# Kernel tuning notes

Hardware: AMD Instinct MI355X
Metric: run time of the kernel (lower is better)

Reference implementation:

```python
import jax
import jax.numpy as jnp
import numpy as np
from jax import lax


def hard_sigmoid(x):
    # keras hard_sigmoid: clip(0.2*x + 0.5, 0, 1)
    return jnp.clip(0.2 * x + 0.5, 0.0, 1.0)


def setup_inputs() -> dict:
    key = jax.random.key(0)
    k1, k2, k3 = jax.random.split(key, 3)
    B, T, H, W, C = 8, 16, 256, 256, 3
    F, K = 36, 5
    states_in = jax.random.normal(k1, (B, T, H, W, C), dtype=jnp.float32)
    Wx = jax.random.normal(k2, (K, K, C, 4 * F), dtype=jnp.float32) * 0.05
    Wh = jax.random.normal(k3, (K, K, F, 4 * F), dtype=jnp.float32) * 0.05
    b = jnp.zeros((4 * F,), dtype=jnp.float32)
    return {"states_in": states_in, "Wx": Wx, "Wh": Wh, "b": b}


def reference(states_in, Wx, Wh, b):
    # ConvLSTM2D(filters=36, kernel=5, strides=(4,4), padding='valid') + Flatten
    B, T, H, W, C = states_in.shape
    F = Wh.shape[2]
    dn = ("NHWC", "HWIO", "NHWC")

    # Precompute strided input convs for all timesteps in one big conv (batched over B*T)
    x = states_in.reshape(B * T, H, W, C)
    xconv = lax.conv_general_dilated(x, Wx, (4, 4), "VALID", dimension_numbers=dn) + b
    Ho, Wo = xconv.shape[1], xconv.shape[2]  # (256-5)//4+1 = 63
    xconv = xconv.reshape(B, T, Ho, Wo, 4 * F).transpose(1, 0, 2, 3, 4)  # time-major

    def step(carry, xt):
        h, c = carry
        # recurrent conv: strides 1, SAME padding (keras ConvLSTM2D behavior)
        hconv = lax.conv_general_dilated(h, Wh, (1, 1), "SAME", dimension_numbers=dn)
        z = xt + hconv
        zi, zf, zc, zo = jnp.split(z, 4, axis=-1)  # keras gate order i,f,c,o
        i = hard_sigmoid(zi)
        f = hard_sigmoid(zf)
        o = hard_sigmoid(zo)
        c_new = f * c + i * jnp.tanh(zc)
        h_new = o * jnp.tanh(c_new)
        return (h_new, c_new), None

    h0 = jnp.zeros((B, Ho, Wo, F), dtype=states_in.dtype)
    (h, c), _ = lax.scan(step, (h0, h0), xconv)
    return h.reshape(B, -1)  # Flatten -> (B, Ho*Wo*F)
```

## Files before the change

### kernel.cpp

```cpp
#include <hip/hip_runtime.h>


typedef _Float16 f16;
typedef __attribute__((ext_vector_type(8))) _Float16 f16x8;
typedef __attribute__((ext_vector_type(4))) float f32x4;

#define TPB 256

#define H_SH_OFF   0
#define X_SH_OFF   28944
#define W2_SH_OFF  43136
#define W_SH_OFF   100736
#define Z_SH_OFF   28944
#define LDS_BYTES  160640

#define WHP_GRAN_PER_SLICE 1872
#define W_BUF_USH 14976

union Cv8 { ushort4 u4[2]; uint4 q; f16x8 h8; };
union Cvh { f16 h; ushort u; };
union Cv2 { f16 h[2]; uint u; };

__device__ inline f16x8 ld8_lds(const ushort* p) {
  Cv8 c; c.u4[0] = *(const ushort4*)p; c.u4[1] = *(const ushort4*)(p + 4);
  return c.h8;
}
__device__ inline f16x8 ld16_lds(const ushort* p) {
  Cv8 c; c.q = *(const uint4*)p; return c.h8;
}
__device__ inline ushort f2us(float v) { Cvh c; c.h = (f16)v; return c.u; }

typedef const __attribute__((address_space(1))) uint guint;
typedef __attribute__((address_space(3))) uint luint;
__device__ inline void gload_lds16(const void* gp, void* lp) {
  __builtin_amdgcn_global_load_lds((guint*)gp, (luint*)lp, 16, 0, 0);
}

__device__ inline float tanh_fast(float x) {
  float e = __expf(2.f * x);
  return 1.f - 2.f * __builtin_amdgcn_rcpf(e + 1.f);
}

__global__ void prep_weights(const float* __restrict__ Wx, const float* __restrict__ Wh,
                             const float* __restrict__ bb,
                             ushort* __restrict__ whp, ushort* __restrict__ wxp,
                             float* __restrict__ bperm) {
  int i = blockIdx.x * 256 + threadIdx.x;
  if (i < 149760) {
    int kk = i % 104; int rest = i / 104;
    int np = rest % 144; int s = rest / 144;
    int kh = s >> 1, hf = s & 1;
    int k = hf * 96 + kk;
    float v = 0.f;
    if (kk < 96 && k < 180) {
      int kw = k / 36, c = k - kw * 36;
      int fq = np >> 4, g = (np >> 2) & 3, fr = np & 3;
      int n = g * 36 + fq * 4 + fr;
      v = Wh[(((kh * 5 + kw) * 36 + c) * 144) + n];
    }
    whp[i] = f2us(v);
  } else if (i < 178560) {
    int e = i - 149760;
    int kk2 = e % 40; int rest = e / 40;
    int np = rest % 144; int kh2 = rest / 144;
    float v = 0.f;
    if (kk2 < 15) {
      int kw = kk2 / 3, cin = kk2 - kw * 3;
      int fq = np >> 4, g = (np >> 2) & 3, fr = np & 3;
      int n = g * 36 + fq * 4 + fr;
      v = Wx[(((kh2 * 5 + kw) * 3 + cin) * 144) + n];
    }
    wxp[e] = f2us(v);
  } else if (i < 178704) {
    int np = i - 178560;
    int fq = np >> 4, g = (np >> 2) & 3, fr = np & 3;
    bperm[np] = bb[g * 36 + fq * 4 + fr];
  }
}

template<int S, int FQ0>
__device__ void x_chunks(f32x4 (&acc)[4][5], const ushort* x_sh, const ushort* w2_sh,
                         int mh, int lane) {
  const int l16 = lane & 15, lg = lane >> 4;
#pragma unroll
  for (int kh2 = 0; kh2 < 5; ++kh2) {
    f16x8 a[4];
#pragma unroll
    for (int r = 0; r < 4; ++r)
      a[r] = ld8_lds(x_sh + (mh * 4 + kh2) * 788 + (r * 16 + l16) * 12 + lg * 8);
#pragma unroll
    for (int s = 0; s < S; ++s) {
      f16x8 bf = ld16_lds(w2_sh + (kh2 * 144 + (FQ0 + s) * 16 + l16) * 40 + lg * 8);
#pragma unroll
      for (int r = 0; r < 4; ++r)
        acc[r][s] = __builtin_amdgcn_mfma_f32_16x16x32_f16(a[r], bf, acc[r][s], 0, 0, 0);
    }
  }
}

template<int S, int FQ0>
__device__ void h_chunks(f32x4 (&acc)[4][5], const ushort* h_sh, const ushort* wbuf,
                         int kh, int hf, int mh, int lane) {
  const int l16 = lane & 15, lg = lane >> 4;
  const ushort* hrow = h_sh + (mh + kh) * 2412;
#pragma unroll
  for (int cc = 0; cc < 3; ++cc) {
    const int k0 = hf * 96 + cc * 32;
    f16x8 a[4];
#pragma unroll
    for (int r = 0; r < 4; ++r)
      a[r] = ld8_lds(hrow + (r * 16 + l16) * 36 + k0 + lg * 8);
#pragma unroll
    for (int s = 0; s < S; ++s) {
      f16x8 bf = ld16_lds(wbuf + ((FQ0 + s) * 16 + l16) * 104 + cc * 32 + lg * 8);
#pragma unroll
      for (int r = 0; r < 4; ++r)
        acc[r][s] = __builtin_amdgcn_mfma_f32_16x16x32_f16(a[r], bf, acc[r][s], 0, 0, 0);
    }
  }
}

template<int S, int FQ0>
__device__ void z_write(const f32x4 (&acc)[4][5], float* z_sh, int mh, int lane) {
  const int l16 = lane & 15, lg = lane >> 4;
#pragma unroll
  for (int r = 0; r < 4; ++r)
#pragma unroll
    for (int s = 0; s < S; ++s)
#pragma unroll
      for (int j = 0; j < 4; ++j)
        z_sh[(mh * 64 + r * 16 + lg * 4 + j) * 148 + (FQ0 + s) * 16 + l16] = acc[r][s][j];
}

__device__ inline void stage_wh_slice(const ushort* whp, int slice, ushort* dstbuf, int tid) {
  const uint4* src = (const uint4*)whp + (size_t)slice * WHP_GRAN_PER_SLICE;
#pragma unroll
  for (int k = 0; k < 8; ++k) {
    int g = tid + k * 256;
    if (g < WHP_GRAN_PER_SLICE)
      gload_lds16(src + g, (char*)dstbuf + (size_t)g * 16);
  }
}

__global__ __launch_bounds__(TPB, 1)
void convlstm_step(const float* __restrict__ x_all, int t,
                   const f16* __restrict__ h_prev, f16* __restrict__ h_next,
                   float* __restrict__ c_st,
                   const ushort* __restrict__ whp, const ushort* __restrict__ wxp,
                   const float* __restrict__ bperm,
                   float* __restrict__ out, int flags) {
  extern __shared__ char smem[];
  ushort* h_sh  = (ushort*)(smem + H_SH_OFF);
  ushort* x_sh  = (ushort*)(smem + X_SH_OFF);
  ushort* w2_sh = (ushort*)(smem + W2_SH_OFF);
  ushort* w_sh  = (ushort*)(smem + W_SH_OFF);
  float*  z_sh  = (float*)(smem + Z_SH_OFF);

  const int tid = threadIdx.x;
  const int lane = tid & 63, wave = tid >> 6;
  const int mh = wave >> 1, nh = wave & 1;
  const int y0 = blockIdx.x * 2, b = blockIdx.y;
  const bool first = (flags & 1) != 0, last = (flags & 2) != 0;

  {
    const uint4* src = (const uint4*)wxp;
#pragma unroll
    for (int k = 0; k < 15; ++k) {
      int g = tid + k * 256;
      if (g < 3600) gload_lds16(src + g, (char*)w2_sh + (size_t)g * 16);
    }
  }
  if (!first) stage_wh_slice(whp, 0, w_sh, tid);

  {
    const float* xrow0 = x_all + (size_t)(b * 16 + t) * 196608;
    uint* xs32 = (uint*)x_sh;
#pragma unroll
    for (int k = 0; k < 7; ++k) {
      int g = tid + k * 256;
      if (g < 1728) {
        int row = g / 192, e = g - row * 192;
        int yi = y0 * 4 + row;
        float4 v = make_float4(0.f, 0.f, 0.f, 0.f);
        if (yi < 256) v = *(const float4*)(xrow0 + yi * 768 + e * 4);
        Cv2 c0, c1;
        c0.h[0] = (f16)v.x; c0.h[1] = (f16)v.y;
        c1.h[0] = (f16)v.z; c1.h[1] = (f16)v.w;
        xs32[row * 394 + e * 2]     = c0.u;
        xs32[row * 394 + e * 2 + 1] = c1.u;
      }
    }
    if (tid < 90) {
      int row = tid / 10, u = 384 + (tid - (tid / 10) * 10);
      xs32[row * 394 + u] = 0;
    }
  }
  if (!first) {
    const uint2* src = (const uint2*)h_prev;
    uint2* hs = (uint2*)h_sh;
#pragma unroll
    for (int k = 0; k < 15; ++k) {
      int g = tid + k * 256;
      if (g < 3618) {
        int row = g / 603, u2 = g - row * 603;
        int hy = y0 - 2 + row;
        uint2 val = make_uint2(0, 0);
        if (hy >= 0 && hy < 63 && u2 >= 18 && u2 < 585)
          val = src[(size_t)(b * 63 + hy) * 567 + (u2 - 18)];
        hs[g] = val;
      }
    }
  }
  __syncthreads();

  f32x4 acc[4][5];
#pragma unroll
  for (int r = 0; r < 4; ++r)
#pragma unroll
    for (int s = 0; s < 5; ++s) acc[r][s] = (f32x4)(0.f);

  if (nh == 0) x_chunks<5, 0>(acc, x_sh, w2_sh, mh, lane);
  else         x_chunks<4, 5>(acc, x_sh, w2_sh, mh, lane);

  if (!first) {
#pragma unroll 1
    for (int s = 0; s < 10; ++s) {
      if (s < 9)
        stage_wh_slice(whp, s + 1, w_sh + ((s + 1) & 1) * W_BUF_USH, tid);
      const ushort* wbuf = w_sh + (s & 1) * W_BUF_USH;
      if (nh == 0) h_chunks<5, 0>(acc, h_sh, wbuf, s >> 1, s & 1, mh, lane);
      else         h_chunks<4, 5>(acc, h_sh, wbuf, s >> 1, s & 1, mh, lane);
      __syncthreads();
    }
  }

  __syncthreads();
  if (nh == 0) z_write<5, 0>(acc, z_sh, mh, lane);
  else         z_write<4, 5>(acc, z_sh, mh, lane);
  __syncthreads();

#pragma unroll 1
  for (int it = 0; it < 18; ++it) {
    int u = tid + it * 256;
    int x_sub = u / 36, f = u - x_sub * 36;
    int x = x_sub & 63, y = y0 + (x_sub >> 6);
    if (x < 63 && y < 63) {
      int cb = (f >> 2) * 16 + (f & 3);
      const float* zr = z_sh + x_sub * 148;
      float zi = zr[cb]      + bperm[cb];
      float zf = zr[cb + 4]  + bperm[cb + 4];
      float zc = zr[cb + 8]  + bperm[cb + 8];
      float zo = zr[cb + 12] + bperm[cb + 12];
      float gi = fminf(fmaxf(0.2f * zi + 0.5f, 0.f), 1.f);
      float gf = fminf(fmaxf(0.2f * zf + 0.5f, 0.f), 1.f);
      float go = fminf(fmaxf(0.2f * zo + 0.5f, 0.f), 1.f);
      float tc = tanh_fast(zc);
      size_t idx = (size_t)((b * 63 + y) * 63 + x) * 36 + f;
      float cold = first ? 0.f : c_st[idx];
      float cn = gf * cold + gi * tc;
      float hn = go * tanh_fast(cn);
      c_st[idx] = cn;
      h_next[idx] = (f16)hn;
      if (last) out[(size_t)b * 142884 + ((y * 63 + x) * 36 + f)] = hn;
    }
  }
}

extern "C" void kernel_launch(void* const* d_in, const int* in_sizes, int n_in,
                              void* d_out, int out_size, void* d_ws, size_t ws_size,
                              hipStream_t stream) {
  (void)in_sizes; (void)n_in; (void)out_size; (void)ws_size;
  const float* states = (const float*)d_in[0];
  const float* Wx = (const float*)d_in[1];
  const float* Wh = (const float*)d_in[2];
  const float* bb = (const float*)d_in[3];
  float* out = (float*)d_out;
  char* ws = (char*)d_ws;

  ushort* whp   = (ushort*)(ws + 0);
  ushort* wxp   = (ushort*)(ws + 299520);
  float*  bperm = (float*)(ws + 357120);
  f16*    hb0   = (f16*)(ws + 357696);
  f16*    hb1   = (f16*)(ws + 2643840);
  float*  c_st  = (float*)(ws + 4929984);

  hipFuncSetAttribute((const void*)convlstm_step,
                      hipFuncAttributeMaxDynamicSharedMemorySize, LDS_BYTES);

  prep_weights<<<699, 256, 0, stream>>>(Wx, Wh, bb, whp, wxp, bperm);
  for (int t = 0; t < 16; ++t) {
    int flags = (t == 0 ? 1 : 0) | (t == 15 ? 2 : 0);
    f16* hp = (t & 1) ? hb1 : hb0;
    f16* hn = (t & 1) ? hb0 : hb1;
    convlstm_step<<<dim3(32, 8), TPB, LDS_BYTES, stream>>>(
        states, t, hp, hn, c_st, whp, wxp, bperm, out, flags);
  }
}
```

Measured before the change: 614.9 us.

## Fuse all timesteps into one persistent cooperative kernel with split-K waves

Replaces the 16 per-timestep launches with a single cooperative kernel that loops over time and uses a grid-wide sync between steps. Block size doubles to 512 so two wave groups split the K reduction, and their partial accumulators are summed through LDS. The Wh staging is rebuilt as a six-chunk ring of 32-wide K chunks, the x conv switches to 16x16x16 MFMA with a tighter weight layout, and the bias is cached in LDS. This removes per-step launch overhead and idle tails, at the cost of grid-sync latency and an extra LDS reduction pass.

```diff
diff --git a/kernel.cpp b/kernel.cpp
--- a/kernel.cpp
+++ b/kernel.cpp
@@ -1,23 +1,29 @@
 #include <hip/hip_runtime.h>
+#include <hip/hip_cooperative_groups.h>
+
+namespace cg = cooperative_groups;
 
 
 typedef _Float16 f16;
+typedef __attribute__((ext_vector_type(4))) _Float16 f16x4;
 typedef __attribute__((ext_vector_type(8))) _Float16 f16x8;
 typedef __attribute__((ext_vector_type(4))) float f32x4;
 
-#define TPB 256
+#define TPB 512
 
 #define H_SH_OFF   0
 #define X_SH_OFF   28944
-#define W2_SH_OFF  43136
-#define W_SH_OFF   100736
-#define Z_SH_OFF   28944
-#define LDS_BYTES  160640
-
-#define WHP_GRAN_PER_SLICE 1872
-#define W_BUF_USH 14976
+#define RING_OFF   43136
+#define W2_SH_OFF  112256
+#define BP_OFF     141056
+#define LDS_BYTES  141632
+#define Z_SH_OFF   0
+
+#define CHUNK_USH 5760
+#define CHUNK_U4  720
 
 union Cv8 { ushort4 u4[2]; uint4 q; f16x8 h8; };
+union Cv4 { ushort4 u; f16x4 h; };
 union Cvh { f16 h; ushort u; };
 union Cv2 { f16 h[2]; uint u; };
 
@@ -27,6 +33,9 @@
 }
 __device__ inline f16x8 ld16_lds(const ushort* p) {
   Cv8 c; c.q = *(const uint4*)p; return c.h8;
+}
+__device__ inline f16x4 ld4_lds(const ushort* p) {
+  Cv4 c; c.u = *(const ushort4*)p; return c.h;
 }
 __device__ inline ushort f2us(float v) { Cvh c; c.h = (f16)v; return c.u; }
 
@@ -46,223 +55,247 @@
                              ushort* __restrict__ whp, ushort* __restrict__ wxp,
                              float* __restrict__ bperm) {
   int i = blockIdx.x * 256 + threadIdx.x;
-  if (i < 149760) {
-    int kk = i % 104; int rest = i / 104;
-    int np = rest % 144; int s = rest / 144;
-    int kh = s >> 1, hf = s & 1;
-    int k = hf * 96 + kk;
+  if (i < 172800) {
+    int j = i % 40; int rest = i / 40;
+    int np = rest % 144; int ck = rest / 144;
+    int kh = ck / 6, cc6 = ck - kh * 6;
+    int k = cc6 * 32 + j;
     float v = 0.f;
-    if (kk < 96 && k < 180) {
+    if (j < 32 && k < 180) {
       int kw = k / 36, c = k - kw * 36;
       int fq = np >> 4, g = (np >> 2) & 3, fr = np & 3;
       int n = g * 36 + fq * 4 + fr;
       v = Wh[(((kh * 5 + kw) * 36 + c) * 144) + n];
     }
     whp[i] = f2us(v);
-  } else if (i < 178560) {
-    int e = i - 149760;
-    int kk2 = e % 40; int rest = e / 40;
+  } else if (i < 187200) {
+    int e = i - 172800;
+    int j = e % 20; int rest = e / 20;
     int np = rest % 144; int kh2 = rest / 144;
     float v = 0.f;
-    if (kk2 < 15) {
-      int kw = kk2 / 3, cin = kk2 - kw * 3;
+    if (j < 15) {
+      int kw = j / 3, cin = j - kw * 3;
       int fq = np >> 4, g = (np >> 2) & 3, fr = np & 3;
       int n = g * 36 + fq * 4 + fr;
       v = Wx[(((kh2 * 5 + kw) * 3 + cin) * 144) + n];
     }
     wxp[e] = f2us(v);
-  } else if (i < 178704) {
-    int np = i - 178560;
+  } else if (i < 187344) {
+    int np = i - 187200;
     int fq = np >> 4, g = (np >> 2) & 3, fr = np & 3;
     bperm[np] = bb[g * 36 + fq * 4 + fr];
   }
 }
 
+template<int S, int FQ0, int K0, int K1>
+__device__ void x_conv(f32x4 (&acc)[4][5], const ushort* x_sh, const ushort* w2,
+                       int mh, int l16, int lg) {
+#pragma unroll
+  for (int kh2 = K0; kh2 < K1; ++kh2) {
+    f16x4 a[4];
+#pragma unroll
+    for (int r = 0; r < 4; ++r)
+      a[r] = ld4_lds(x_sh + (mh * 4 + kh2) * 788 + (r * 16 + l16) * 12 + lg * 4);
+#pragma unroll
+    for (int s = 0; s < S; ++s) {
+      f16x4 bf = ld4_lds(w2 + (kh2 * 144 + (FQ0 + s) * 16 + l16) * 20 + lg * 4);
+#pragma unroll
+      for (int r = 0; r < 4; ++r)
+        acc[r][s] = __builtin_amdgcn_mfma_f32_16x16x16f16(a[r], bf, acc[r][s], 0, 0, 0);
+    }
+  }
+}
+
 template<int S, int FQ0>
-__device__ void x_chunks(f32x4 (&acc)[4][5], const ushort* x_sh, const ushort* w2_sh,
-                         int mh, int lane) {
+__device__ void h_phase(f32x4 (&acc)[4][5], const ushort* hrow, const ushort* wbuf,
+                        int k0, int l16, int lg) {
+  f16x8 a[4];
+#pragma unroll
+  for (int r = 0; r < 4; ++r)
+    a[r] = ld8_lds(hrow + (r * 16 + l16) * 36 + k0 + lg * 8);
+#pragma unroll
+  for (int s = 0; s < S; ++s) {
+    f16x8 bf = ld16_lds(wbuf + ((FQ0 + s) * 16 + l16) * 40 + lg * 8);
+#pragma unroll
+    for (int r = 0; r < 4; ++r)
+      acc[r][s] = __builtin_amdgcn_mfma_f32_16x16x32_f16(a[r], bf, acc[r][s], 0, 0, 0);
+  }
+}
+
+template<int S, int FQ0, bool ADD>
+__device__ void z_out(const f32x4 (&acc)[4][5], float* z_sh, int mh, int l16, int lg) {
+#pragma unroll
+  for (int r = 0; r < 4; ++r)
+#pragma unroll
+    for (int s = 0; s < S; ++s)
+#pragma unroll
+      for (int j = 0; j < 4; ++j) {
+        float* p = &z_sh[(mh * 64 + r * 16 + lg * 4 + j) * 148 + (FQ0 + s) * 16 + l16];
+        if (ADD) *p += acc[r][s][j]; else *p = acc[r][s][j];
+      }
+}
+
+__global__ __launch_bounds__(TPB, 2)
+void convlstm_all(const float* __restrict__ x_all,
+                  const ushort* __restrict__ whp, const ushort* __restrict__ wxp,
+                  const float* __restrict__ bperm,
+                  f16* __restrict__ hb0, f16* __restrict__ hb1,
+                  float* __restrict__ c_st, float* __restrict__ out) {
+  extern __shared__ char smem[];
+  ushort* h_sh = (ushort*)(smem + H_SH_OFF);
+  ushort* x_sh = (ushort*)(smem + X_SH_OFF);
+  ushort* ring = (ushort*)(smem + RING_OFF);
+  ushort* w2   = (ushort*)(smem + W2_SH_OFF);
+  float*  bp_sh = (float*)(smem + BP_OFF);
+  float*  z_sh  = (float*)(smem + Z_SH_OFF);
+
+  cg::grid_group gg = cg::this_grid();
+
+  const int tid = threadIdx.x;
+  const int lane = tid & 63, w = tid >> 6;
+  const int kq = w >> 2, mh = (w >> 1) & 1, nh = w & 1;
   const int l16 = lane & 15, lg = lane >> 4;
-#pragma unroll
-  for (int kh2 = 0; kh2 < 5; ++kh2) {
-    f16x8 a[4];
-#pragma unroll
-    for (int r = 0; r < 4; ++r)
-      a[r] = ld8_lds(x_sh + (mh * 4 + kh2) * 788 + (r * 16 + l16) * 12 + lg * 8);
-#pragma unroll
-    for (int s = 0; s < S; ++s) {
-      f16x8 bf = ld16_lds(w2_sh + (kh2 * 144 + (FQ0 + s) * 16 + l16) * 40 + lg * 8);
-#pragma unroll
-      for (int r = 0; r < 4; ++r)
-        acc[r][s] = __builtin_amdgcn_mfma_f32_16x16x32_f16(a[r], bf, acc[r][s], 0, 0, 0);
-    }
-  }
-}
-
-template<int S, int FQ0>
-__device__ void h_chunks(f32x4 (&acc)[4][5], const ushort* h_sh, const ushort* wbuf,
-                         int kh, int hf, int mh, int lane) {
-  const int l16 = lane & 15, lg = lane >> 4;
-  const ushort* hrow = h_sh + (mh + kh) * 2412;
-#pragma unroll
-  for (int cc = 0; cc < 3; ++cc) {
-    const int k0 = hf * 96 + cc * 32;
-    f16x8 a[4];
-#pragma unroll
-    for (int r = 0; r < 4; ++r)
-      a[r] = ld8_lds(hrow + (r * 16 + l16) * 36 + k0 + lg * 8);
-#pragma unroll
-    for (int s = 0; s < S; ++s) {
-      f16x8 bf = ld16_lds(wbuf + ((FQ0 + s) * 16 + l16) * 104 + cc * 32 + lg * 8);
-#pragma unroll
-      for (int r = 0; r < 4; ++r)
-        acc[r][s] = __builtin_amdgcn_mfma_f32_16x16x32_f16(a[r], bf, acc[r][s], 0, 0, 0);
-    }
-  }
-}
-
-template<int S, int FQ0>
-__device__ void z_write(const f32x4 (&acc)[4][5], float* z_sh, int mh, int lane) {
-  const int l16 = lane & 15, lg = lane >> 4;
-#pragma unroll
-  for (int r = 0; r < 4; ++r)
-#pragma unroll
-    for (int s = 0; s < S; ++s)
-#pragma unroll
-      for (int j = 0; j < 4; ++j)
-        z_sh[(mh * 64 + r * 16 + lg * 4 + j) * 148 + (FQ0 + s) * 16 + l16] = acc[r][s][j];
-}
-
-__device__ inline void stage_wh_slice(const ushort* whp, int slice, ushort* dstbuf, int tid) {
-  const uint4* src = (const uint4*)whp + (size_t)slice * WHP_GRAN_PER_SLICE;
-#pragma unroll
-  for (int k = 0; k < 8; ++k) {
-    int g = tid + k * 256;
-    if (g < WHP_GRAN_PER_SLICE)
-      gload_lds16(src + g, (char*)dstbuf + (size_t)g * 16);
-  }
-}
-
-__global__ __launch_bounds__(TPB, 1)
-void convlstm_step(const float* __restrict__ x_all, int t,
-                   const f16* __restrict__ h_prev, f16* __restrict__ h_next,
-                   float* __restrict__ c_st,
-                   const ushort* __restrict__ whp, const ushort* __restrict__ wxp,
-                   const float* __restrict__ bperm,
-                   float* __restrict__ out, int flags) {
-  extern __shared__ char smem[];
-  ushort* h_sh  = (ushort*)(smem + H_SH_OFF);
-  ushort* x_sh  = (ushort*)(smem + X_SH_OFF);
-  ushort* w2_sh = (ushort*)(smem + W2_SH_OFF);
-  ushort* w_sh  = (ushort*)(smem + W_SH_OFF);
-  float*  z_sh  = (float*)(smem + Z_SH_OFF);
-
-  const int tid = threadIdx.x;
-  const int lane = tid & 63, wave = tid >> 6;
-  const int mh = wave >> 1, nh = wave & 1;
-  const int y0 = blockIdx.x * 2, b = blockIdx.y;
-  const bool first = (flags & 1) != 0, last = (flags & 2) != 0;
+  const int bid = blockIdx.x;
+  const int b = bid & 7;
+  const int y0 = (bid >> 3) * 2;
 
   {
     const uint4* src = (const uint4*)wxp;
 #pragma unroll
-    for (int k = 0; k < 15; ++k) {
-      int g = tid + k * 256;
-      if (g < 3600) gload_lds16(src + g, (char*)w2_sh + (size_t)g * 16);
-    }
-  }
-  if (!first) stage_wh_slice(whp, 0, w_sh, tid);
-
-  {
-    const float* xrow0 = x_all + (size_t)(b * 16 + t) * 196608;
-    uint* xs32 = (uint*)x_sh;
-#pragma unroll
-    for (int k = 0; k < 7; ++k) {
-      int g = tid + k * 256;
-      if (g < 1728) {
-        int row = g / 192, e = g - row * 192;
-        int yi = y0 * 4 + row;
-        float4 v = make_float4(0.f, 0.f, 0.f, 0.f);
-        if (yi < 256) v = *(const float4*)(xrow0 + yi * 768 + e * 4);
-        Cv2 c0, c1;
-        c0.h[0] = (f16)v.x; c0.h[1] = (f16)v.y;
-        c1.h[0] = (f16)v.z; c1.h[1] = (f16)v.w;
-        xs32[row * 394 + e * 2]     = c0.u;
-        xs32[row * 394 + e * 2 + 1] = c1.u;
-      }
-    }
-    if (tid < 90) {
-      int row = tid / 10, u = 384 + (tid - (tid / 10) * 10);
-      xs32[row * 394 + u] = 0;
-    }
-  }
-  if (!first) {
-    const uint2* src = (const uint2*)h_prev;
-    uint2* hs = (uint2*)h_sh;
-#pragma unroll
-    for (int k = 0; k < 15; ++k) {
-      int g = tid + k * 256;
-      if (g < 3618) {
-        int row = g / 603, u2 = g - row * 603;
-        int hy = y0 - 2 + row;
-        uint2 val = make_uint2(0, 0);
-        if (hy >= 0 && hy < 63 && u2 >= 18 && u2 < 585)
-          val = src[(size_t)(b * 63 + hy) * 567 + (u2 - 18)];
-        hs[g] = val;
-      }
-    }
-  }
-  __syncthreads();
-
-  f32x4 acc[4][5];
-#pragma unroll
-  for (int r = 0; r < 4; ++r)
-#pragma unroll
-    for (int s = 0; s < 5; ++s) acc[r][s] = (f32x4)(0.f);
-
-  if (nh == 0) x_chunks<5, 0>(acc, x_sh, w2_sh, mh, lane);
-  else         x_chunks<4, 5>(acc, x_sh, w2_sh, mh, lane);
-
-  if (!first) {
+    for (int k = 0; k < 4; ++k) {
+      int g = tid + k * 512;
+      if (g < 1800) gload_lds16(src + g, (char*)w2 + (size_t)g * 16);
+    }
+    if (tid < 144) bp_sh[tid] = bperm[tid];
+  }
+
 #pragma unroll 1
-    for (int s = 0; s < 10; ++s) {
-      if (s < 9)
-        stage_wh_slice(whp, s + 1, w_sh + ((s + 1) & 1) * W_BUF_USH, tid);
-      const ushort* wbuf = w_sh + (s & 1) * W_BUF_USH;
-      if (nh == 0) h_chunks<5, 0>(acc, h_sh, wbuf, s >> 1, s & 1, mh, lane);
-      else         h_chunks<4, 5>(acc, h_sh, wbuf, s >> 1, s & 1, mh, lane);
+  for (int t = 0; t < 16; ++t) {
+    const f16* hp = (t & 1) ? hb1 : hb0;
+    f16* hn = (t & 1) ? hb0 : hb1;
+    const bool first = (t == 0), last = (t == 15);
+
+    if (!first) {
+      const uint4* src = (const uint4*)whp;
+#pragma unroll
+      for (int k = 0; k < 6; ++k) {
+        int g = tid + k * 512;
+        if (g < 4 * CHUNK_U4) gload_lds16(src + g, (char*)ring + (size_t)g * 16);
+      }
+    }
+    {
+      const float* xr = x_all + (size_t)(b * 16 + t) * 196608;
+      uint* xs = (uint*)x_sh;
+#pragma unroll
+      for (int k = 0; k < 4; ++k) {
+        int g = tid + k * 512;
+        if (g < 1728) {
+          int row = g / 192, e = g - row * 192;
+          int yi = y0 * 4 + row;
+          float4 v = make_float4(0.f, 0.f, 0.f, 0.f);
+          if (yi < 256) v = *(const float4*)(xr + yi * 768 + e * 4);
+          Cv2 c0, c1;
+          c0.h[0] = (f16)v.x; c0.h[1] = (f16)v.y;
+          c1.h[0] = (f16)v.z; c1.h[1] = (f16)v.w;
+          xs[row * 394 + e * 2]     = c0.u;
+          xs[row * 394 + e * 2 + 1] = c1.u;
+        }
+      }
+      if (tid < 90) {
+        int row = tid / 10, u = 384 + (tid - (tid / 10) * 10);
+        xs[row * 394 + u] = 0;
+      }
+    }
+    if (!first) {
+      const uint2* src = (const uint2*)hp;
+      uint2* hs = (uint2*)h_sh;
+#pragma unroll
+      for (int k = 0; k < 8; ++k) {
+        int g = tid + k * 512;
+        if (g < 3618) {
+          int row = g / 603, u2 = g - row * 603;
+          int hy = y0 - 2 + row;
+          uint2 val = make_uint2(0, 0);
+          if (hy >= 0 && hy < 63 && u2 >= 18 && u2 < 585)
+            val = src[(size_t)(b * 63 + hy) * 567 + (u2 - 18)];
+          hs[g] = val;
+        }
+      }
+    }
+    __syncthreads();
+
+    f32x4 acc[4][5];
+#pragma unroll
+    for (int r = 0; r < 4; ++r)
+#pragma unroll
+      for (int s = 0; s < 5; ++s) acc[r][s] = (f32x4)(0.f);
+
+    if (nh == 0) { if (kq == 0) x_conv<5, 0, 0, 3>(acc, x_sh, w2, mh, l16, lg);
+                   else         x_conv<5, 0, 3, 5>(acc, x_sh, w2, mh, l16, lg); }
+    else         { if (kq == 0) x_conv<4, 5, 0, 3>(acc, x_sh, w2, mh, l16, lg);
+                   else         x_conv<4, 5, 3, 5>(acc, x_sh, w2, mh, l16, lg); }
+
+    if (!first) {
+#pragma unroll 1
+      for (int q = 0; q < 5; ++q) {
+        const ushort* hrow = h_sh + (mh + q) * 2412;
+#pragma unroll
+        for (int r3 = 0; r3 < 3; ++r3) {
+          int nc = 6 * q + 2 * r3 + 4;
+          if (nc < 30) {
+            const uint4* src = (const uint4*)whp + (size_t)nc * CHUNK_U4;
+            char* dst = (char*)ring + ((2 * r3 + 4) % 6) * (CHUNK_USH * 2);
+#pragma unroll
+            for (int k = 0; k < 3; ++k) {
+              int g = tid + k * 512;
+              if (g < 2 * CHUNK_U4) gload_lds16(src + g, dst + (size_t)g * 16);
+            }
+          }
+          const int cc6 = 2 * r3 + kq;
+          const ushort* wbuf = ring + cc6 * CHUNK_USH;
+          if (nh == 0) h_phase<5, 0>(acc, hrow, wbuf, cc6 * 32, l16, lg);
+          else         h_phase<4, 5>(acc, hrow, wbuf, cc6 * 32, l16, lg);
+          __syncthreads();
+        }
+      }
+    } else {
       __syncthreads();
     }
-  }
-
-  __syncthreads();
-  if (nh == 0) z_write<5, 0>(acc, z_sh, mh, lane);
-  else         z_write<4, 5>(acc, z_sh, mh, lane);
-  __syncthreads();
+
+    if (kq == 0) { if (nh == 0) z_out<5, 0, false>(acc, z_sh, mh, l16, lg);
+                   else         z_out<4, 5, false>(acc, z_sh, mh, l16, lg); }
+    __syncthreads();
+    if (kq == 1) { if (nh == 0) z_out<5, 0, true>(acc, z_sh, mh, l16, lg);
+                   else         z_out<4, 5, true>(acc, z_sh, mh, l16, lg); }
+    __syncthreads();
 
 #pragma unroll 1
-  for (int it = 0; it < 18; ++it) {
-    int u = tid + it * 256;
-    int x_sub = u / 36, f = u - x_sub * 36;
-    int x = x_sub & 63, y = y0 + (x_sub >> 6);
-    if (x < 63 && y < 63) {
-      int cb = (f >> 2) * 16 + (f & 3);
-      const float* zr = z_sh + x_sub * 148;
-      float zi = zr[cb]      + bperm[cb];
-      float zf = zr[cb + 4]  + bperm[cb + 4];
-      float zc = zr[cb + 8]  + bperm[cb + 8];
-      float zo = zr[cb + 12] + bperm[cb + 12];
-      float gi = fminf(fmaxf(0.2f * zi + 0.5f, 0.f), 1.f);
-      float gf = fminf(fmaxf(0.2f * zf + 0.5f, 0.f), 1.f);
-      float go = fminf(fmaxf(0.2f * zo + 0.5f, 0.f), 1.f);
-      float tc = tanh_fast(zc);
-      size_t idx = (size_t)((b * 63 + y) * 63 + x) * 36 + f;
-      float cold = first ? 0.f : c_st[idx];
-      float cn = gf * cold + gi * tc;
-      float hn = go * tanh_fast(cn);
-      c_st[idx] = cn;
-      h_next[idx] = (f16)hn;
-      if (last) out[(size_t)b * 142884 + ((y * 63 + x) * 36 + f)] = hn;
-    }
+    for (int it = 0; it < 9; ++it) {
+      int u = tid + it * 512;
+      int x_sub = u / 36, f = u - x_sub * 36;
+      int x = x_sub & 63, y = y0 + (x_sub >> 6);
+      if (x < 63 && y < 63) {
+        int cb = (f >> 2) * 16 + (f & 3);
+        const float* zr = z_sh + x_sub * 148;
+        float zi = zr[cb]      + bp_sh[cb];
+        float zf = zr[cb + 4]  + bp_sh[cb + 4];
+        float zc = zr[cb + 8]  + bp_sh[cb + 8];
+        float zo = zr[cb + 12] + bp_sh[cb + 12];
+        float gi = fminf(fmaxf(0.2f * zi + 0.5f, 0.f), 1.f);
+        float gf = fminf(fmaxf(0.2f * zf + 0.5f, 0.f), 1.f);
+        float go = fminf(fmaxf(0.2f * zo + 0.5f, 0.f), 1.f);
+        float tc = tanh_fast(zc);
+        size_t idx = (size_t)((b * 63 + y) * 63 + x) * 36 + f;
+        float cold = first ? 0.f : c_st[idx];
+        float cn = gf * cold + gi * tc;
+        float hnv = go * tanh_fast(cn);
+        c_st[idx] = cn;
+        hn[idx] = (f16)hnv;
+        if (last) out[(size_t)b * 142884 + ((y * 63 + x) * 36 + f)] = hnv;
+      }
+    }
+
+    if (!last) { __threadfence(); gg.sync(); }
   }
 }
 
@@ -278,21 +311,20 @@
   char* ws = (char*)d_ws;
 
   ushort* whp   = (ushort*)(ws + 0);
-  ushort* wxp   = (ushort*)(ws + 299520);
-  float*  bperm = (float*)(ws + 357120);
-  f16*    hb0   = (f16*)(ws + 357696);
-  f16*    hb1   = (f16*)(ws + 2643840);
-  float*  c_st  = (float*)(ws + 4929984);
-
-  hipFuncSetAttribute((const void*)convlstm_step,
+  ushort* wxp   = (ushort*)(ws + 345600);
+  float*  bperm = (float*)(ws + 374400);
+  f16*    hb0   = (f16*)(ws + 374976);
+  f16*    hb1   = (f16*)(ws + 2661120);
+  float*  c_st  = (float*)(ws + 4947264);
+
+  (void)hipFuncSetAttribute((const void*)convlstm_all,
                       hipFuncAttributeMaxDynamicSharedMemorySize, LDS_BYTES);
 
-  prep_weights<<<699, 256, 0, stream>>>(Wx, Wh, bb, whp, wxp, bperm);
-  for (int t = 0; t < 16; ++t) {
-    int flags = (t == 0 ? 1 : 0) | (t == 15 ? 2 : 0);
-    f16* hp = (t & 1) ? hb1 : hb0;
-    f16* hn = (t & 1) ? hb0 : hb1;
-    convlstm_step<<<dim3(32, 8), TPB, LDS_BYTES, stream>>>(
-        states, t, hp, hn, c_st, whp, wxp, bperm, out, flags);
-  }
-}
+  prep_weights<<<732, 256, 0, stream>>>(Wx, Wh, bb, whp, wxp, bperm);
+
+  const float* xa = states;
+  void* args[] = { (void*)&xa, (void*)&whp, (void*)&wxp, (void*)&bperm,
+                   (void*)&hb0, (void*)&hb1, (void*)&c_st, (void*)&out };
+  (void)hipLaunchCooperativeKernel((void*)convlstm_all, dim3(256), dim3(TPB),
+                             args, LDS_BYTES, stream);
+}
```

Result: slower. 1.752 ms (+184.9%).
